# Optimization experiments

Measured on AMD Instinct MI355X. Metric: run time of the kernel, lower is better.

Reference implementation:

```python
import jax, jax.numpy as jnp
import numpy as np

B_TRIALS = 64   # n_trials
DZ = 512        # latent / network dim
DU = 16         # input dim
DX = 256        # observation dim
T = 1000        # time steps
DECAY = 0.9
G = np.sqrt(2.0)


def setup_inputs() -> dict:
    key = jax.random.key(0)
    k0, k1, k2, k3, k4 = jax.random.split(key, 5)
    z0 = jax.random.normal(k0, (B_TRIALS, DZ), jnp.float32)
    v = jax.random.normal(k1, (B_TRIALS, DU, T), jnp.float32)
    # W ~ (1-decay) * g / sqrt(dz) * N(0,1), per Transition_FullRank init
    W = ((1.0 - DECAY) * G / np.sqrt(DZ)) * jax.random.normal(k2, (DZ, DZ), jnp.float32)
    # Wu: uniform init scaled by 1/sqrt(du)
    Wu = (jax.random.uniform(k3, (DZ, DU), jnp.float32) * 2.0 - 1.0) / np.sqrt(DU)
    h = jnp.zeros((DZ,), jnp.float32)
    # decay_param = log(-log(decay))
    decay_param = jnp.full((1,), np.log(-np.log(DECAY)), jnp.float32)
    # Affine_observation: B ~ sqrt(2/(dz+dv)) * N(0,1), dv=0
    B_obs = np.sqrt(2.0 / DZ) * jax.random.normal(k4, (DZ, DX), jnp.float32)
    Bias = jnp.zeros((DX,), jnp.float32)
    return dict(z0=z0, v=v, W=W, Wu=Wu, h=h, decay_param=decay_param,
                B_obs=B_obs, Bias=Bias)


def reference(z0, v, W, Wu, h, decay_param, B_obs, Bias):
    # decay = exp(-exp(decay_param))
    decay = jnp.exp(-jnp.exp(decay_param[0]))
    v_seq = jnp.transpose(v, (2, 0, 1))  # [T, B, du]

    def step(z, vt):
        # z' = decay*z + W @ relu(z - h) + Wu @ v_t  (per trial)
        z_new = decay * z + jax.nn.relu(z - h) @ W.T + vt @ Wu.T
        return z_new, z_new

    _, zs = jax.lax.scan(step, z0, v_seq)      # [T, B, dz]
    zs = jnp.transpose(zs, (1, 2, 0))          # [B, dz, T]
    # Affine_observation (identity nonlinearity): einsum('zx,bzt->bxt') + bias
    x = jnp.einsum('zx,bzt->bxt', B_obs, zs) + Bias[None, :, None]
    return x
```

## Files before the change

### kernel.cpp

```cpp
#include <hip/hip_runtime.h>

#define DZc 512
#define Bc  64
#define Tc  1000
#define DUc 16
#define DXc 256
#define AROW 552


typedef __attribute__((ext_vector_type(4))) float f32x4;
typedef __attribute__((ext_vector_type(8))) short s16x8;
typedef __attribute__((ext_vector_type(4))) unsigned u32x4;

__device__ __forceinline__ unsigned short f2bf(float x) {
  unsigned u = __builtin_bit_cast(unsigned, x);
  u = u + 0x7FFFu + ((u >> 16) & 1u);
  return (unsigned short)(u >> 16);
}
__device__ __forceinline__ float bf2f(unsigned short u) {
  unsigned x = ((unsigned)u) << 16;
  return __builtin_bit_cast(float, x);
}
__device__ __forceinline__ unsigned pack_pair(float val) {
  unsigned bf = f2bf(val);
  unsigned sw = (unsigned)__builtin_amdgcn_mov_dpp((int)bf, 0xB1, 0xF, 0xF, true);
  return bf | (sw << 16);
}

__global__ void pack_w_kernel(const float* __restrict__ W,
                              const float* __restrict__ Wu,
                              unsigned short* __restrict__ Wp) {
  int d = blockIdx.x * 256 + threadIdx.x;
  int j = d & 7, l = (d >> 3) & 63, nt = (d >> 9) & 31, kt = d >> 14;
  int n = nt * 16 + (l & 15);
  int k = kt * 32 + ((l >> 4) << 3) + j;
  float val = (k < DZc) ? W[n * DZc + k] : Wu[n * DUc + (k & 15)];
  Wp[d] = f2bf(val);
}

__global__ void pack_b_kernel(const float* __restrict__ B,
                              unsigned short* __restrict__ Bp) {
  int d = blockIdx.x * 256 + threadIdx.x;
  int j = d & 7, l = (d >> 3) & 63, nt = (d >> 9) & 15, kt = d >> 13;
  int n = nt * 16 + (l & 15);
  int k = kt * 32 + ((l >> 4) << 3) + j;
  Bp[d] = f2bf(B[k * DXc + n]);
}

__global__ __launch_bounds__(512, 2) void rnn_rec_kernel(
    const float* __restrict__ z0, const float* __restrict__ v,
    const float* __restrict__ h, const float* __restrict__ dp,
    const unsigned short* __restrict__ Wp, unsigned short* __restrict__ zs,
    unsigned int* __restrict__ flags) {
  __shared__ __align__(16) unsigned short abuf[2][16][AROW];

  const int bid = blockIdx.x;
  const int g = bid & 7;
  const int s = bid >> 3;
  if (g >= 4) return;
  const int tid = threadIdx.x;
  const int lane = tid & 63;
  const int w = tid >> 6;
  const int l15 = lane & 15;
  const int lg = lane >> 4;
  const int b0 = g * 16;
  const int nbase = s * 256 + w * 32;
  const int s8 = s * 8, o8 = 8 - s8;

  s16x8 wr[34];
#pragma unroll
  for (int i = 0; i < 17; ++i) {
    int kt = (i < 8) ? (s8 + i) : (i == 8) ? 16 : (o8 + (i - 9));
#pragma unroll
    for (int ntl = 0; ntl < 2; ++ntl) {
      int nt = s * 16 + w * 2 + ntl;
      wr[i * 2 + ntl] =
          *(const s16x8*)(Wp + ((size_t)((kt * 32 + nt) * 64 + lane)) * 8);
    }
  }

  float hreg[2];
  f32x4 acc[2];
#pragma unroll
  for (int ntl = 0; ntl < 2; ++ntl) {
    hreg[ntl] = h[nbase + ntl * 16 + l15];
#pragma unroll
    for (int r = 0; r < 4; ++r)
      acc[ntl][r] = z0[(size_t)(b0 + lg * 4 + r) * DZc + nbase + ntl * 16 + l15];
  }
  const float decay = expf(-expf(dp[0]));

  const int ptrial = tid >> 5;
  const int koff = (tid & 31) * 8;
  const int pk = (1 - s) * 256 + koff;
  float hpart[8];
#pragma unroll
  for (int j = 0; j < 8; ++j) hpart[j] = h[pk + j];

  const int du = tid & 15, trr = tid >> 4;
  const size_t vbase = ((size_t)(b0 + trr) * DUc + du) * Tc;
  float vcur = (tid < 256) ? v[vbase] : 0.f;

#pragma unroll
  for (int half = 0; half < 2; ++half) {
    int kk = half * 256 + koff;
    const float* zp = z0 + (size_t)(b0 + ptrial) * DZc + kk;
    s16x8 ov;
#pragma unroll
    for (int j = 0; j < 8; ++j) {
      float av = zp[j] - h[kk + j];
      ov[j] = (short)f2bf(av > 0.f ? av : 0.f);
    }
    *(s16x8*)&abuf[0][ptrial][kk] = ov;
  }
  if (tid < 256) {
    unsigned short hi = f2bf(vcur);
    abuf[0][trr][512 + du] = hi;
    abuf[0][trr][528 + du] = f2bf(vcur - bf2f(hi));
  }

  unsigned int* myflag = flags + (g * 2 + s);
  unsigned int* pflag = flags + (g * 2 + (s ^ 1));
  unsigned* zs32 = (unsigned*)zs;

  int p = 0;
  for (int t = 0; t < Tc; ++t) {
    u32x4 pz4 = {0, 0, 0, 0};
    if (t > 0) {
      int iters = 0;
      while (__hip_atomic_load(pflag, __ATOMIC_RELAXED,
                               __HIP_MEMORY_SCOPE_AGENT) < (unsigned)t) {
        __builtin_amdgcn_s_sleep(2);
        if (++iters > (1 << 22)) break;
      }
      asm volatile("" ::: "memory");
      pz4 = *(const u32x4*)(zs32 +
            ((size_t)(t - 1) * Bc + b0 + ptrial) * 256 + (pk >> 1));
    }
    float vnext = (tid < 256) ? v[vbase + (t + 1 < Tc ? t + 1 : Tc - 1)] : 0.f;
#pragma unroll
    for (int ntl = 0; ntl < 2; ++ntl)
#pragma unroll
      for (int r = 0; r < 4; ++r) acc[ntl][r] *= decay;

    asm volatile("s_waitcnt lgkmcnt(0)\n\ts_barrier" ::: "memory");

#pragma unroll
    for (int i = 0; i < 9; ++i) {
      int kt = (i < 8) ? (s8 + i) : 16;
      s16x8 af = *(const s16x8*)&abuf[p][l15][kt * 32 + lg * 8];
      acc[0] = __builtin_amdgcn_mfma_f32_16x16x32_bf16(af, wr[i * 2 + 0], acc[0], 0, 0, 0);
      acc[1] = __builtin_amdgcn_mfma_f32_16x16x32_bf16(af, wr[i * 2 + 1], acc[1], 0, 0, 0);
    }

    if (t > 0) {
      s16x8 ov;
#pragma unroll
      for (int j2 = 0; j2 < 4; ++j2) {
        unsigned wd = pz4[j2];
        float alo = bf2f((unsigned short)(wd & 0xFFFFu)) - hpart[j2 * 2];
        float ahi = bf2f((unsigned short)(wd >> 16)) - hpart[j2 * 2 + 1];
        ov[j2 * 2] = (short)f2bf(alo > 0.f ? alo : 0.f);
        ov[j2 * 2 + 1] = (short)f2bf(ahi > 0.f ? ahi : 0.f);
      }
      *(s16x8*)&abuf[p][ptrial][pk] = ov;
    }
    asm volatile("s_waitcnt lgkmcnt(0)\n\ts_barrier" ::: "memory");

#pragma unroll
    for (int i = 0; i < 8; ++i) {
      int kt = o8 + i;
      s16x8 af = *(const s16x8*)&abuf[p][l15][kt * 32 + lg * 8];
      acc[0] = __builtin_amdgcn_mfma_f32_16x16x32_bf16(af, wr[18 + i * 2], acc[0], 0, 0, 0);
      acc[1] = __builtin_amdgcn_mfma_f32_16x16x32_bf16(af, wr[19 + i * 2], acc[1], 0, 0, 0);
    }

    const size_t zrow0 = (size_t)t * Bc + b0 + lg * 4;
#pragma unroll
    for (int ntl = 0; ntl < 2; ++ntl)
#pragma unroll
      for (int r = 0; r < 4; ++r) {
        unsigned wdz = pack_pair(acc[ntl][r]);
        if (!(lane & 1))
          __hip_atomic_store(
              zs32 + (zrow0 + r) * 256 + (nbase >> 1) + ntl * 8 + (l15 >> 1),
              wdz, __ATOMIC_RELAXED, __HIP_MEMORY_SCOPE_AGENT);
      }

#pragma unroll
    for (int ntl = 0; ntl < 2; ++ntl)
#pragma unroll
      for (int r = 0; r < 4; ++r) {
        float av = acc[ntl][r] - hreg[ntl];
        unsigned wda = pack_pair(av > 0.f ? av : 0.f);
        if (!(lane & 1))
          *(unsigned*)&abuf[p ^ 1][lg * 4 + r][nbase + ntl * 16 + (l15 & ~1)] = wda;
      }
    if (tid < 256) {
      unsigned short hi = f2bf(vnext);
      abuf[p ^ 1][trr][512 + du] = hi;
      abuf[p ^ 1][trr][528 + du] = f2bf(vnext - bf2f(hi));
    }

    asm volatile("s_waitcnt vmcnt(0)" ::: "memory");
    __builtin_amdgcn_s_barrier();
    if (tid == 0)
      __hip_atomic_store(myflag, (unsigned)(t + 1), __ATOMIC_RELAXED,
                         __HIP_MEMORY_SCOPE_AGENT);
    p ^= 1;
    vcur = vnext;
  }
}

__global__ __launch_bounds__(256, 1) void rnn_proj_kernel(
    const unsigned short* __restrict__ zs, const unsigned short* __restrict__ Bp,
    const float* __restrict__ Bias, float* __restrict__ x) {
  const int wg = blockIdx.x;
  const int b = wg / 63;
  const int tbase = (wg % 63) * 16;
  const int tid = threadIdx.x;
  const int lane = tid & 63;
  const int w = tid >> 6;
  const int l15 = lane & 15, lg = lane >> 4;

  const int trow = tbase + l15;
  const int trc = trow < Tc ? trow : Tc - 1;
  const unsigned short* abase = zs + ((size_t)trc * Bc + b) * DZc + lg * 8;
  const s16x8 zz = {0, 0, 0, 0, 0, 0, 0, 0};

  f32x4 acc[4];
#pragma unroll
  for (int n = 0; n < 4; ++n)
#pragma unroll
    for (int e = 0; e < 4; ++e) acc[n][e] = 0.f;

#pragma unroll
  for (int kt = 0; kt < 16; ++kt) {
    s16x8 af = *(const s16x8*)(abase + kt * 32);
    af = (trow < Tc) ? af : zz;
#pragma unroll
    for (int n = 0; n < 4; ++n) {
      s16x8 bf = *(const s16x8*)(Bp + (size_t)((kt * 16 + w * 4 + n) * 64 + lane) * 8);
      acc[n] = __builtin_amdgcn_mfma_f32_16x16x32_bf16(af, bf, acc[n], 0, 0, 0);
    }
  }

  const int t = tbase + lg * 4;
  if (t < Tc) {
#pragma unroll
    for (int n = 0; n < 4; ++n) {
      int xo = (w * 4 + n) * 16 + l15;
      float bias = Bias[xo];
      f32x4 val = acc[n];
#pragma unroll
      for (int e = 0; e < 4; ++e) val[e] += bias;
      *(f32x4*)(x + ((size_t)b * DXc + xo) * Tc + t) = val;
    }
  }
}

extern "C" void kernel_launch(void* const* d_in, const int* in_sizes, int n_in,
                              void* d_out, int out_size, void* d_ws, size_t ws_size,
                              hipStream_t stream) {
  const float* z0   = (const float*)d_in[0];
  const float* v    = (const float*)d_in[1];
  const float* W    = (const float*)d_in[2];
  const float* Wu   = (const float*)d_in[3];
  const float* h    = (const float*)d_in[4];
  const float* dp   = (const float*)d_in[5];
  const float* Bo   = (const float*)d_in[6];
  const float* Bias = (const float*)d_in[7];
  float* x = (float*)d_out;

  unsigned short* Wp = (unsigned short*)d_ws;
  unsigned short* Bp = Wp + 278528;
  unsigned short* zs = Bp + 131072;
  unsigned int* flags = (unsigned int*)(zs + 32768000);

  hipMemsetAsync(flags, 0, 8 * sizeof(unsigned int), stream);
  pack_w_kernel<<<1088, 256, 0, stream>>>(W, Wu, Wp);
  pack_b_kernel<<<512, 256, 0, stream>>>(Bo, Bp);
  rnn_rec_kernel<<<16, 512, 0, stream>>>(z0, v, h, dp, Wp, zs, flags);
  rnn_proj_kernel<<<4032, 256, 0, stream>>>(zs, Bp, Bias, x);
}
```

Baseline: 2.009 ms.

## Halve recurrent block to 4 waves, each computing four output tiles

```diff
diff --git a/kernel.cpp b/kernel.cpp
--- a/kernel.cpp
+++ b/kernel.cpp
@@ -47,7 +47,7 @@
   Bp[d] = f2bf(B[k * DXc + n]);
 }
 
-__global__ __launch_bounds__(512, 2) void rnn_rec_kernel(
+__global__ __launch_bounds__(256, 1) void rnn_rec_kernel(
     const float* __restrict__ z0, const float* __restrict__ v,
     const float* __restrict__ h, const float* __restrict__ dp,
     const unsigned short* __restrict__ Wp, unsigned short* __restrict__ zs,
@@ -64,25 +64,25 @@
   const int l15 = lane & 15;
   const int lg = lane >> 4;
   const int b0 = g * 16;
-  const int nbase = s * 256 + w * 32;
+  const int nbase = s * 256 + w * 64;
   const int s8 = s * 8, o8 = 8 - s8;
 
-  s16x8 wr[34];
+  s16x8 wr[68];
 #pragma unroll
   for (int i = 0; i < 17; ++i) {
     int kt = (i < 8) ? (s8 + i) : (i == 8) ? 16 : (o8 + (i - 9));
 #pragma unroll
-    for (int ntl = 0; ntl < 2; ++ntl) {
-      int nt = s * 16 + w * 2 + ntl;
-      wr[i * 2 + ntl] =
+    for (int ntl = 0; ntl < 4; ++ntl) {
+      int nt = s * 16 + w * 4 + ntl;
+      wr[i * 4 + ntl] =
           *(const s16x8*)(Wp + ((size_t)((kt * 32 + nt) * 64 + lane)) * 8);
     }
   }
 
-  float hreg[2];
-  f32x4 acc[2];
-#pragma unroll
-  for (int ntl = 0; ntl < 2; ++ntl) {
+  float hreg[4];
+  f32x4 acc[4];
+#pragma unroll
+  for (int ntl = 0; ntl < 4; ++ntl) {
     hreg[ntl] = h[nbase + ntl * 16 + l15];
 #pragma unroll
     for (int r = 0; r < 4; ++r)
@@ -90,7 +90,7 @@
   }
   const float decay = expf(-expf(dp[0]));
 
-  const int ptrial = tid >> 5;
+  const int pA = tid >> 5;
   const int koff = (tid & 31) * 8;
   const int pk = (1 - s) * 256 + koff;
   float hpart[8];
@@ -99,25 +99,29 @@
 
   const int du = tid & 15, trr = tid >> 4;
   const size_t vbase = ((size_t)(b0 + trr) * DUc + du) * Tc;
-  float vcur = (tid < 256) ? v[vbase] : 0.f;
-
-#pragma unroll
-  for (int half = 0; half < 2; ++half) {
-    int kk = half * 256 + koff;
-    const float* zp = z0 + (size_t)(b0 + ptrial) * DZc + kk;
-    s16x8 ov;
-#pragma unroll
-    for (int j = 0; j < 8; ++j) {
-      float av = zp[j] - h[kk + j];
-      ov[j] = (short)f2bf(av > 0.f ? av : 0.f);
-    }
-    *(s16x8*)&abuf[0][ptrial][kk] = ov;
-  }
-  if (tid < 256) {
+  float vcur = v[vbase];
+
+#pragma unroll
+  for (int half = 0; half < 2; ++half)
+#pragma unroll
+    for (int dtr = 0; dtr < 2; ++dtr) {
+      int trial = pA + dtr * 8;
+      int kk = half * 256 + koff;
+      const float* zp = z0 + (size_t)(b0 + trial) * DZc + kk;
+      s16x8 ov;
+#pragma unroll
+      for (int j = 0; j < 8; ++j) {
+        float av = zp[j] - h[kk + j];
+        ov[j] = (short)f2bf(av > 0.f ? av : 0.f);
+      }
+      *(s16x8*)&abuf[0][trial][kk] = ov;
+    }
+  {
     unsigned short hi = f2bf(vcur);
     abuf[0][trr][512 + du] = hi;
     abuf[0][trr][528 + du] = f2bf(vcur - bf2f(hi));
   }
+  asm volatile("s_waitcnt lgkmcnt(0)\n\ts_barrier" ::: "memory");
 
   unsigned int* myflag = flags + (g * 2 + s);
   unsigned int* pflag = flags + (g * 2 + (s ^ 1));
@@ -125,7 +129,7 @@
 
   int p = 0;
   for (int t = 0; t < Tc; ++t) {
-    u32x4 pz4 = {0, 0, 0, 0};
+    u32x4 pzA = {0, 0, 0, 0}, pzB = {0, 0, 0, 0};
     if (t > 0) {
       int iters = 0;
       while (__hip_atomic_load(pflag, __ATOMIC_RELAXED,
@@ -134,50 +138,58 @@
         if (++iters > (1 << 22)) break;
       }
       asm volatile("" ::: "memory");
-      pz4 = *(const u32x4*)(zs32 +
-            ((size_t)(t - 1) * Bc + b0 + ptrial) * 256 + (pk >> 1));
-    }
-    float vnext = (tid < 256) ? v[vbase + (t + 1 < Tc ? t + 1 : Tc - 1)] : 0.f;
-#pragma unroll
-    for (int ntl = 0; ntl < 2; ++ntl)
+      const unsigned* src =
+          zs32 + ((size_t)(t - 1) * Bc + b0 + pA) * 256 + (pk >> 1);
+      pzA = *(const u32x4*)src;
+      pzB = *(const u32x4*)(src + 8 * 256);
+    }
+    float vnext = v[vbase + (t + 1 < Tc ? t + 1 : Tc - 1)];
+#pragma unroll
+    for (int ntl = 0; ntl < 4; ++ntl)
 #pragma unroll
       for (int r = 0; r < 4; ++r) acc[ntl][r] *= decay;
-
-    asm volatile("s_waitcnt lgkmcnt(0)\n\ts_barrier" ::: "memory");
 
 #pragma unroll
     for (int i = 0; i < 9; ++i) {
       int kt = (i < 8) ? (s8 + i) : 16;
       s16x8 af = *(const s16x8*)&abuf[p][l15][kt * 32 + lg * 8];
-      acc[0] = __builtin_amdgcn_mfma_f32_16x16x32_bf16(af, wr[i * 2 + 0], acc[0], 0, 0, 0);
-      acc[1] = __builtin_amdgcn_mfma_f32_16x16x32_bf16(af, wr[i * 2 + 1], acc[1], 0, 0, 0);
+#pragma unroll
+      for (int ntl = 0; ntl < 4; ++ntl)
+        acc[ntl] = __builtin_amdgcn_mfma_f32_16x16x32_bf16(
+            af, wr[i * 4 + ntl], acc[ntl], 0, 0, 0);
     }
 
     if (t > 0) {
-      s16x8 ov;
-#pragma unroll
-      for (int j2 = 0; j2 < 4; ++j2) {
-        unsigned wd = pz4[j2];
-        float alo = bf2f((unsigned short)(wd & 0xFFFFu)) - hpart[j2 * 2];
-        float ahi = bf2f((unsigned short)(wd >> 16)) - hpart[j2 * 2 + 1];
-        ov[j2 * 2] = (short)f2bf(alo > 0.f ? alo : 0.f);
-        ov[j2 * 2 + 1] = (short)f2bf(ahi > 0.f ? ahi : 0.f);
-      }
-      *(s16x8*)&abuf[p][ptrial][pk] = ov;
+#pragma unroll
+      for (int dtr = 0; dtr < 2; ++dtr) {
+        u32x4 pz4 = dtr ? pzB : pzA;
+        s16x8 ov;
+#pragma unroll
+        for (int j2 = 0; j2 < 4; ++j2) {
+          unsigned wd = pz4[j2];
+          float alo = bf2f((unsigned short)(wd & 0xFFFFu)) - hpart[j2 * 2];
+          float ahi = bf2f((unsigned short)(wd >> 16)) - hpart[j2 * 2 + 1];
+          ov[j2 * 2] = (short)f2bf(alo > 0.f ? alo : 0.f);
+          ov[j2 * 2 + 1] = (short)f2bf(ahi > 0.f ? ahi : 0.f);
+        }
+        *(s16x8*)&abuf[p][pA + dtr * 8][pk] = ov;
+      }
     }
     asm volatile("s_waitcnt lgkmcnt(0)\n\ts_barrier" ::: "memory");
 
 #pragma unroll
-    for (int i = 0; i < 8; ++i) {
-      int kt = o8 + i;
+    for (int i = 9; i < 17; ++i) {
+      int kt = o8 + (i - 9);
       s16x8 af = *(const s16x8*)&abuf[p][l15][kt * 32 + lg * 8];
-      acc[0] = __builtin_amdgcn_mfma_f32_16x16x32_bf16(af, wr[18 + i * 2], acc[0], 0, 0, 0);
-      acc[1] = __builtin_amdgcn_mfma_f32_16x16x32_bf16(af, wr[19 + i * 2], acc[1], 0, 0, 0);
+#pragma unroll
+      for (int ntl = 0; ntl < 4; ++ntl)
+        acc[ntl] = __builtin_amdgcn_mfma_f32_16x16x32_bf16(
+            af, wr[i * 4 + ntl], acc[ntl], 0, 0, 0);
     }
 
     const size_t zrow0 = (size_t)t * Bc + b0 + lg * 4;
 #pragma unroll
-    for (int ntl = 0; ntl < 2; ++ntl)
+    for (int ntl = 0; ntl < 4; ++ntl)
 #pragma unroll
       for (int r = 0; r < 4; ++r) {
         unsigned wdz = pack_pair(acc[ntl][r]);
@@ -188,7 +200,7 @@
       }
 
 #pragma unroll
-    for (int ntl = 0; ntl < 2; ++ntl)
+    for (int ntl = 0; ntl < 4; ++ntl)
 #pragma unroll
       for (int r = 0; r < 4; ++r) {
         float av = acc[ntl][r] - hreg[ntl];
@@ -196,14 +208,13 @@
         if (!(lane & 1))
           *(unsigned*)&abuf[p ^ 1][lg * 4 + r][nbase + ntl * 16 + (l15 & ~1)] = wda;
       }
-    if (tid < 256) {
+    {
       unsigned short hi = f2bf(vnext);
       abuf[p ^ 1][trr][512 + du] = hi;
       abuf[p ^ 1][trr][528 + du] = f2bf(vnext - bf2f(hi));
     }
 
-    asm volatile("s_waitcnt vmcnt(0)" ::: "memory");
-    __builtin_amdgcn_s_barrier();
+    asm volatile("s_waitcnt vmcnt(0) lgkmcnt(0)\n\ts_barrier" ::: "memory");
     if (tid == 0)
       __hip_atomic_store(myflag, (unsigned)(t + 1), __ATOMIC_RELAXED,
                          __HIP_MEMORY_SCOPE_AGENT);
@@ -280,6 +291,6 @@
   hipMemsetAsync(flags, 0, 8 * sizeof(unsigned int), stream);
   pack_w_kernel<<<1088, 256, 0, stream>>>(W, Wu, Wp);
   pack_b_kernel<<<512, 256, 0, stream>>>(Bo, Bp);
-  rnn_rec_kernel<<<16, 512, 0, stream>>>(z0, v, h, dp, Wp, zs, flags);
+  rnn_rec_kernel<<<16, 256, 0, stream>>>(z0, v, h, dp, Wp, zs, flags);
   rnn_proj_kernel<<<4032, 256, 0, stream>>>(zs, Bp, Bias, x);
 }
```

Result: slower. 3.033 ms (+50.9%).

## Use per-wave flags and overlap partner wait with local MFMA work

Applied to the files above, without the earlier changes.

```diff
diff --git a/kernel.cpp b/kernel.cpp
--- a/kernel.cpp
+++ b/kernel.cpp
@@ -21,10 +21,14 @@
   unsigned x = ((unsigned)u) << 16;
   return __builtin_bit_cast(float, x);
 }
-__device__ __forceinline__ unsigned pack_pair(float val) {
-  unsigned bf = f2bf(val);
-  unsigned sw = (unsigned)__builtin_amdgcn_mov_dpp((int)bf, 0xB1, 0xF, 0xF, true);
-  return bf | (sw << 16);
+__device__ __forceinline__ unsigned cvt_pk_bf16(float lo, float hi) {
+  unsigned r;
+  asm("v_cvt_pk_bf16_f32 %0, %1, %2" : "=v"(r) : "v"(lo), "v"(hi));
+  return r;
+}
+__device__ __forceinline__ float dpp_swap1(float x) {
+  int r = __builtin_amdgcn_mov_dpp(__builtin_bit_cast(int, x), 0xB1, 0xF, 0xF, true);
+  return __builtin_bit_cast(float, r);
 }
 
 __global__ void pack_w_kernel(const float* __restrict__ W,
@@ -118,84 +122,111 @@
     abuf[0][trr][512 + du] = hi;
     abuf[0][trr][528 + du] = f2bf(vcur - bf2f(hi));
   }
-
-  unsigned int* myflag = flags + (g * 2 + s);
-  unsigned int* pflag = flags + (g * 2 + (s ^ 1));
+  asm volatile("s_waitcnt lgkmcnt(0)\n\ts_barrier" ::: "memory");
+
+  unsigned int* myflag = flags + ((g * 2 + s) * 8 + w) * 16;
+  const unsigned int* pflag =
+      flags + ((g * 2 + (s ^ 1)) * 8 + ((tid & 31) >> 2)) * 16;
   unsigned* zs32 = (unsigned*)zs;
 
   int p = 0;
   for (int t = 0; t < Tc; ++t) {
-    u32x4 pz4 = {0, 0, 0, 0};
+    float vnext = (tid < 256) ? v[vbase + (t + 1 < Tc ? t + 1 : Tc - 1)] : 0.f;
+
+#pragma unroll
+    for (int ntl = 0; ntl < 2; ++ntl)
+#pragma unroll
+      for (int r = 0; r < 4; ++r) acc[ntl][r] *= decay;
+
+#pragma unroll
+    for (int ii = 0; ii < 5; ++ii) {
+      int i = (ii == 0) ? 8 : (ii - 1);
+      int kt = (i == 8) ? 16 : (s8 + i);
+      s16x8 af = *(const s16x8*)&abuf[p][l15][kt * 32 + lg * 8];
+      acc[0] = __builtin_amdgcn_mfma_f32_16x16x32_bf16(af, wr[i * 2 + 0], acc[0], 0, 0, 0);
+      acc[1] = __builtin_amdgcn_mfma_f32_16x16x32_bf16(af, wr[i * 2 + 1], acc[1], 0, 0, 0);
+    }
+
+    unsigned pz0 = 0, pz1 = 0, pz2 = 0, pz3 = 0;
     if (t > 0) {
       int iters = 0;
-      while (__hip_atomic_load(pflag, __ATOMIC_RELAXED,
-                               __HIP_MEMORY_SCOPE_AGENT) < (unsigned)t) {
-        __builtin_amdgcn_s_sleep(2);
+      while (true) {
+        unsigned fv = __hip_atomic_load(pflag, __ATOMIC_RELAXED,
+                                        __HIP_MEMORY_SCOPE_AGENT);
+        if (__all((int)(fv >= (unsigned)t))) break;
+        __builtin_amdgcn_s_sleep(1);
         if (++iters > (1 << 22)) break;
       }
       asm volatile("" ::: "memory");
-      pz4 = *(const u32x4*)(zs32 +
-            ((size_t)(t - 1) * Bc + b0 + ptrial) * 256 + (pk >> 1));
-    }
-    float vnext = (tid < 256) ? v[vbase + (t + 1 < Tc ? t + 1 : Tc - 1)] : 0.f;
-#pragma unroll
-    for (int ntl = 0; ntl < 2; ++ntl)
-#pragma unroll
-      for (int r = 0; r < 4; ++r) acc[ntl][r] *= decay;
-
-    asm volatile("s_waitcnt lgkmcnt(0)\n\ts_barrier" ::: "memory");
-
-#pragma unroll
-    for (int i = 0; i < 9; ++i) {
-      int kt = (i < 8) ? (s8 + i) : 16;
+      const unsigned* src =
+          zs32 + ((size_t)(t - 1) * Bc + b0 + ptrial) * 256 + (pk >> 1);
+      pz0 = __hip_atomic_load(src + 0, __ATOMIC_RELAXED, __HIP_MEMORY_SCOPE_AGENT);
+      pz1 = __hip_atomic_load(src + 1, __ATOMIC_RELAXED, __HIP_MEMORY_SCOPE_AGENT);
+      pz2 = __hip_atomic_load(src + 2, __ATOMIC_RELAXED, __HIP_MEMORY_SCOPE_AGENT);
+      pz3 = __hip_atomic_load(src + 3, __ATOMIC_RELAXED, __HIP_MEMORY_SCOPE_AGENT);
+    }
+
+#pragma unroll
+    for (int i = 4; i < 8; ++i) {
+      int kt = s8 + i;
       s16x8 af = *(const s16x8*)&abuf[p][l15][kt * 32 + lg * 8];
       acc[0] = __builtin_amdgcn_mfma_f32_16x16x32_bf16(af, wr[i * 2 + 0], acc[0], 0, 0, 0);
       acc[1] = __builtin_amdgcn_mfma_f32_16x16x32_bf16(af, wr[i * 2 + 1], acc[1], 0, 0, 0);
     }
 
     if (t > 0) {
-      s16x8 ov;
+      u32x4 av;
+      unsigned pz[4] = {pz0, pz1, pz2, pz3};
 #pragma unroll
       for (int j2 = 0; j2 < 4; ++j2) {
-        unsigned wd = pz4[j2];
-        float alo = bf2f((unsigned short)(wd & 0xFFFFu)) - hpart[j2 * 2];
-        float ahi = bf2f((unsigned short)(wd >> 16)) - hpart[j2 * 2 + 1];
-        ov[j2 * 2] = (short)f2bf(alo > 0.f ? alo : 0.f);
-        ov[j2 * 2 + 1] = (short)f2bf(ahi > 0.f ? ahi : 0.f);
+        unsigned wd = pz[j2];
+        float lo = __builtin_bit_cast(float, wd << 16);
+        float hi = __builtin_bit_cast(float, wd & 0xFFFF0000u);
+        lo = lo - hpart[j2 * 2];
+        hi = hi - hpart[j2 * 2 + 1];
+        lo = lo > 0.f ? lo : 0.f;
+        hi = hi > 0.f ? hi : 0.f;
+        av[j2] = cvt_pk_bf16(lo, hi);
       }
-      *(s16x8*)&abuf[p][ptrial][pk] = ov;
+      *(u32x4*)&abuf[p][ptrial][pk] = av;
     }
     asm volatile("s_waitcnt lgkmcnt(0)\n\ts_barrier" ::: "memory");
 
 #pragma unroll
-    for (int i = 0; i < 8; ++i) {
-      int kt = o8 + i;
+    for (int i = 9; i < 17; ++i) {
+      int kt = o8 + (i - 9);
       s16x8 af = *(const s16x8*)&abuf[p][l15][kt * 32 + lg * 8];
-      acc[0] = __builtin_amdgcn_mfma_f32_16x16x32_bf16(af, wr[18 + i * 2], acc[0], 0, 0, 0);
-      acc[1] = __builtin_amdgcn_mfma_f32_16x16x32_bf16(af, wr[19 + i * 2], acc[1], 0, 0, 0);
+      acc[0] = __builtin_amdgcn_mfma_f32_16x16x32_bf16(af, wr[i * 2 + 0], acc[0], 0, 0, 0);
+      acc[1] = __builtin_amdgcn_mfma_f32_16x16x32_bf16(af, wr[i * 2 + 1], acc[1], 0, 0, 0);
     }
 
     const size_t zrow0 = (size_t)t * Bc + b0 + lg * 4;
 #pragma unroll
-    for (int ntl = 0; ntl < 2; ++ntl)
-#pragma unroll
-      for (int r = 0; r < 4; ++r) {
-        unsigned wdz = pack_pair(acc[ntl][r]);
-        if (!(lane & 1))
-          __hip_atomic_store(
-              zs32 + (zrow0 + r) * 256 + (nbase >> 1) + ntl * 8 + (l15 >> 1),
-              wdz, __ATOMIC_RELAXED, __HIP_MEMORY_SCOPE_AGENT);
+    for (int r = 0; r < 4; ++r) {
+      float d0 = dpp_swap1(acc[0][r]);
+      float d1 = dpp_swap1(acc[1][r]);
+      if (!(lane & 1)) {
+        unsigned c0 = cvt_pk_bf16(acc[0][r], d0);
+        unsigned c1 = cvt_pk_bf16(acc[1][r], d1);
+        unsigned* dst = zs32 + (zrow0 + r) * 256 + (nbase >> 1) + (l15 >> 1);
+        __hip_atomic_store(dst, c0, __ATOMIC_RELAXED, __HIP_MEMORY_SCOPE_AGENT);
+        __hip_atomic_store(dst + 8, c1, __ATOMIC_RELAXED, __HIP_MEMORY_SCOPE_AGENT);
       }
-
-#pragma unroll
-    for (int ntl = 0; ntl < 2; ++ntl)
-#pragma unroll
-      for (int r = 0; r < 4; ++r) {
-        float av = acc[ntl][r] - hreg[ntl];
-        unsigned wda = pack_pair(av > 0.f ? av : 0.f);
-        if (!(lane & 1))
-          *(unsigned*)&abuf[p ^ 1][lg * 4 + r][nbase + ntl * 16 + (l15 & ~1)] = wda;
+    }
+
+#pragma unroll
+    for (int r = 0; r < 4; ++r) {
+      float a0 = acc[0][r] - hreg[0]; a0 = a0 > 0.f ? a0 : 0.f;
+      float a1 = acc[1][r] - hreg[1]; a1 = a1 > 0.f ? a1 : 0.f;
+      float d0 = dpp_swap1(a0);
+      float d1 = dpp_swap1(a1);
+      if (!(lane & 1)) {
+        unsigned c0 = cvt_pk_bf16(a0, d0);
+        unsigned c1 = cvt_pk_bf16(a1, d1);
+        *(unsigned*)&abuf[p ^ 1][lg * 4 + r][nbase + (l15 & ~1)] = c0;
+        *(unsigned*)&abuf[p ^ 1][lg * 4 + r][nbase + 16 + (l15 & ~1)] = c1;
       }
+    }
     if (tid < 256) {
       unsigned short hi = f2bf(vnext);
       abuf[p ^ 1][trr][512 + du] = hi;
@@ -203,10 +234,10 @@
     }
 
     asm volatile("s_waitcnt vmcnt(0)" ::: "memory");
-    __builtin_amdgcn_s_barrier();
-    if (tid == 0)
+    if (lane == 0)
       __hip_atomic_store(myflag, (unsigned)(t + 1), __ATOMIC_RELAXED,
                          __HIP_MEMORY_SCOPE_AGENT);
+    asm volatile("s_waitcnt lgkmcnt(0)\n\ts_barrier" ::: "memory");
     p ^= 1;
     vcur = vnext;
   }
@@ -277,7 +308,7 @@
   unsigned short* zs = Bp + 131072;
   unsigned int* flags = (unsigned int*)(zs + 32768000);
 
-  hipMemsetAsync(flags, 0, 8 * sizeof(unsigned int), stream);
+  hipMemsetAsync(flags, 0, 16 * 8 * 16 * sizeof(unsigned int), stream);
   pack_w_kernel<<<1088, 256, 0, stream>>>(W, Wu, Wp);
   pack_b_kernel<<<512, 256, 0, stream>>>(Bo, Bp);
   rnn_rec_kernel<<<16, 512, 0, stream>>>(z0, v, h, dp, Wp, zs, flags);
```

Result: slower. 2.512 ms (+25.0%).
